# Performance work log

Measured on AMD Instinct MI355X. Metric: run time of the kernel, lower is better.

The kernel has to match this reference:

```python
import jax, jax.numpy as jnp
import numpy as np

NUM_USERS = 100000
NUM_ITEMS = 50000
N_NODES = NUM_USERS + NUM_ITEMS
N_EDGES = 3200000
EMB_DIM = 128
N_LAYERS = 3


def setup_inputs() -> dict:
    key = jax.random.key(0)
    ks = jax.random.split(key, 7)
    # nn.init.normal_(std=0.1) embedding init
    user_emb = jax.random.normal(ks[0], (NUM_USERS, EMB_DIM), dtype=jnp.float32) * 0.1
    item_emb = jax.random.normal(ks[1], (NUM_ITEMS, EMB_DIM), dtype=jnp.float32) * 0.1
    # static normalized adjacency in COO form (values from D^-1/2 A D^-1/2 are positive)
    edge_row = jax.random.randint(ks[2], (N_EDGES,), 0, N_NODES, dtype=jnp.int32)
    edge_col = jax.random.randint(ks[3], (N_EDGES,), 0, N_NODES, dtype=jnp.int32)
    edge_val = jax.random.uniform(ks[4], (N_EDGES,), dtype=jnp.float32)
    users = jax.random.randint(ks[5], (2048,), 0, NUM_USERS, dtype=jnp.int32)
    items = jax.random.randint(ks[6], (2048,), 0, NUM_ITEMS, dtype=jnp.int32)
    return {
        "user_emb": user_emb,
        "item_emb": item_emb,
        "edge_val": edge_val,
        "edge_row": edge_row,
        "edge_col": edge_col,
        "users": users,
        "items": items,
    }


def reference(user_emb, item_emb, edge_val, edge_row, edge_col, users, items):
    # computer(): concat user/item tables -> [N, d]
    all_emb = jnp.concatenate([user_emb, item_emb], axis=0)
    acc = all_emb  # running sum of layer embeddings (fused mean over layers)
    emb = all_emb
    for _ in range(N_LAYERS):
        # sparse.mm(G, emb): per-edge gather, scale, scatter-add
        msg = edge_val[:, None] * emb[edge_col]  # [E, d]
        emb = jax.ops.segment_sum(msg, edge_row, num_segments=N_NODES)
        acc = acc + emb
    light_out = acc / jnp.float32(N_LAYERS + 1)  # mean over stacked layer embeddings
    users_emb = light_out[users]
    items_emb = light_out[NUM_USERS + items]
    # gamma = sum(users_emb * items_emb, dim=1)
    return jnp.sum(users_emb * items_emb, axis=1)
```

## Files before the change

### kernel.cpp

```cpp
#include <hip/hip_runtime.h>

#define D 128
#define NUSERS 100000
#define NITEMS 50000
#define NNODES 150000
#define NEDGES 3200000
#define NSEL 2048
#define NBKT 586
#define PBLK 256
#define EPB (NEDGES / PBLK)
#define MATN (NBKT * PBLK)
#define MB ((MATN + 255) / 256)
#define BCAP 8192
#define INIT_BLKS 2048
#define FLG_BLKS ((NNODES + 255) / 256)
#define SELSET_BLKS ((2 * NSEL + 255) / 256)
#define COLMASK 0x3FFFFu

typedef unsigned int uint_t;
typedef unsigned short ushort_t;

__device__ inline uint_t bf16_rne(float f) {
    uint_t x = __float_as_uint(f);
    return (x + 0x7FFFu + ((x >> 16) & 1u)) >> 16;
}

__device__ inline int block_excl_scan(int v, int* lds, int nw) {
    int lane = threadIdx.x & 63;
    int wid = (int)(threadIdx.x >> 6);
    int x = v;
    #pragma unroll
    for (int off = 1; off < 64; off <<= 1) {
        int y = __shfl_up(x, off);
        if (lane >= off) x += y;
    }
    if (lane == 63) lds[wid] = x;
    __syncthreads();
    if (wid == 0) {
        int s = (lane < nw) ? lds[lane] : 0;
        #pragma unroll
        for (int off = 1; off < 16; off <<= 1) {
            int y = __shfl_up(s, off);
            if (lane >= off) s += y;
        }
        if (lane < nw) lds[lane] = s;
    }
    __syncthreads();
    int waveoff = (wid == 0) ? 0 : lds[wid - 1];
    return waveoff + x - v;
}

__global__ void k_prologue(const int* __restrict__ row, int* __restrict__ mat,
                           const float4* __restrict__ u4, const float4* __restrict__ i4,
                           uint4* __restrict__ cur,
                           int* __restrict__ flags, int* __restrict__ selflag) {
    __shared__ int h[NBKT];
    int blk = blockIdx.x;
    if (blk < PBLK) {
        for (int i = threadIdx.x; i < NBKT; i += 256) h[i] = 0;
        __syncthreads();
        int beg = blk * EPB, end = beg + EPB;
        for (int e = beg + threadIdx.x; e < end; e += 256)
            atomicAdd(&h[row[e] >> 8], 1);
        __syncthreads();
        for (int i = threadIdx.x; i < NBKT; i += 256)
            mat[i * PBLK + blk] = h[i];
    } else if (blk < PBLK + INIT_BLKS) {
        size_t total8 = (size_t)NNODES * D / 8;
        size_t ub8 = (size_t)NUSERS * D / 8;
        size_t stride = (size_t)INIT_BLKS * 256;
        for (size_t i = (size_t)(blk - PBLK) * 256 + threadIdx.x; i < total8; i += stride) {
            const float4* src = (i < ub8) ? &u4[2 * i] : &i4[2 * (i - ub8)];
            float4 a = src[0], b = src[1];
            uint4 o;
            o.x = (bf16_rne(a.y) << 16) | bf16_rne(a.x);
            o.y = (bf16_rne(a.w) << 16) | bf16_rne(a.z);
            o.z = (bf16_rne(b.y) << 16) | bf16_rne(b.x);
            o.w = (bf16_rne(b.w) << 16) | bf16_rne(b.z);
            cur[i] = o;
        }
    } else {
        int i = (blk - PBLK - INIT_BLKS) * 256 + threadIdx.x;
        if (i < NNODES) { flags[i] = 0; selflag[i] = 0; }
    }
}

__global__ void k_blocksum(const int* __restrict__ src, int* __restrict__ bsums, int n) {
    int i = blockIdx.x * 256 + threadIdx.x;
    int v = (i < n) ? src[i] : 0;
    #pragma unroll
    for (int off = 32; off; off >>= 1) v += __shfl_down(v, off);
    __shared__ int lds[4];
    int lane = threadIdx.x & 63, wid = (int)(threadIdx.x >> 6);
    if (lane == 0) lds[wid] = v;
    __syncthreads();
    if (threadIdx.x == 0) bsums[blockIdx.x] = lds[0] + lds[1] + lds[2] + lds[3];
}

__global__ void k_scan2(int* __restrict__ mat, const int* __restrict__ bsums, int n,
                        const int* __restrict__ users, const int* __restrict__ items,
                        int* __restrict__ selflag, int* __restrict__ flags) {
    int b = blockIdx.x;
    if (b >= MB) {
        int idx = (b - MB) * 256 + threadIdx.x;
        if (idx < 2 * NSEL) {
            int node = (idx < NSEL) ? users[idx] : NUSERS + items[idx - NSEL];
            selflag[node] = 1;
            flags[node] = 1;
        }
        return;
    }
    __shared__ int red[4];
    __shared__ int lds[4];
    int lane = threadIdx.x & 63, wid = (int)(threadIdx.x >> 6);
    int s = 0;
    for (int j = threadIdx.x; j < b; j += 256) s += bsums[j];
    #pragma unroll
    for (int off = 32; off; off >>= 1) s += __shfl_down(s, off);
    if (lane == 0) red[wid] = s;
    __syncthreads();
    int base = red[0] + red[1] + red[2] + red[3];
    int i = b * 256 + threadIdx.x;
    int v = (i < n) ? mat[i] : 0;
    int ex = block_excl_scan(v, lds, 4);
    if (i < n) mat[i] = base + ex;
}

__global__ void k_p2(const int* __restrict__ row, const int* __restrict__ col,
                     const float* __restrict__ val, const int* __restrict__ mat,
                     uint_t* __restrict__ t4, ushort_t* __restrict__ tv) {
    __shared__ int cur[NBKT];
    for (int i = threadIdx.x; i < NBKT; i += 256)
        cur[i] = mat[i * PBLK + blockIdx.x];
    __syncthreads();
    int beg = blockIdx.x * EPB, end = beg + EPB;
    for (int e = beg + threadIdx.x; e < end; e += 256) {
        int r = row[e];
        int b = r >> 8;
        int pos = atomicAdd(&cur[b], 1);
        int q = (int)(val[e] * 16384.f + 0.5f);
        if (q > 16383) q = 16383;
        t4[pos] = ((uint_t)(r & 255) << 18) | (uint_t)col[e];
        tv[pos] = (ushort_t)q;
    }
}

__global__ void k_p3(const uint_t* __restrict__ t4, const ushort_t* __restrict__ tv,
                     const int* __restrict__ mat, uint_t* __restrict__ recs,
                     int* __restrict__ row_start,
                     const int* __restrict__ selflag, int* __restrict__ flags) {
    __shared__ uint_t b4[BCAP];
    __shared__ ushort_t bv[BCAP];
    __shared__ int h[256];
    __shared__ int lds[4];
    __shared__ unsigned char selb[256];
    int b = blockIdx.x;
    int beg = mat[b * PBLK];
    int end = (b + 1 < NBKT) ? mat[(b + 1) * PBLK] : NEDGES;
    int n = end - beg;
    int rowid = b * 256 + threadIdx.x;
    h[threadIdx.x] = 0;
    selb[threadIdx.x] = (rowid < NNODES) ? (unsigned char)selflag[rowid] : 0;
    if (n <= BCAP) {
        for (int i = threadIdx.x; i < n; i += 256) { b4[i] = t4[beg + i]; bv[i] = tv[beg + i]; }
        __syncthreads();
        for (int i = threadIdx.x; i < n; i += 256)
            atomicAdd(&h[b4[i] >> 18], 1);
        __syncthreads();
        int ex = block_excl_scan(h[threadIdx.x], lds, 4);
        if (rowid < NNODES) row_start[rowid] = beg + ex;
        if (b == NBKT - 1 && threadIdx.x == 0) row_start[NNODES] = NEDGES;
        h[threadIdx.x] = ex;
        __syncthreads();
        for (int i = threadIdx.x; i < n; i += 256) {
            uint_t a = b4[i];
            int r = (int)(a >> 18);
            uint_t c = a & COLMASK;
            int pos = beg + atomicAdd(&h[r], 1);
            recs[pos] = ((uint_t)bv[i] << 18) | c;
            if (selb[r]) flags[c] = 1;
        }
    } else {
        __syncthreads();
        for (int e = beg + threadIdx.x; e < end; e += 256)
            atomicAdd(&h[t4[e] >> 18], 1);
        __syncthreads();
        int ex = block_excl_scan(h[threadIdx.x], lds, 4);
        if (rowid < NNODES) row_start[rowid] = beg + ex;
        if (b == NBKT - 1 && threadIdx.x == 0) row_start[NNODES] = NEDGES;
        h[threadIdx.x] = ex;
        __syncthreads();
        for (int e = beg + threadIdx.x; e < end; e += 256) {
            uint_t a = t4[e];
            int r = (int)(a >> 18);
            uint_t c = a & COLMASK;
            int pos = beg + atomicAdd(&h[r], 1);
            recs[pos] = ((uint_t)tv[e] << 18) | c;
            if (selb[r]) flags[c] = 1;
        }
    }
}

__global__ void k_spmm_csr(const uint_t* __restrict__ emb, uint_t* __restrict__ outp,
                           const int* __restrict__ row_start,
                           const uint_t* __restrict__ recs,
                           const int* __restrict__ flags, int use_flags) {
    int lane = threadIdx.x & 63;
    int w = (int)((blockIdx.x * blockDim.x + threadIdx.x) >> 6);
    if (w >= NNODES) return;
    if (use_flags && __builtin_amdgcn_readfirstlane(flags[w]) == 0) return;
    int beg = __builtin_amdgcn_readfirstlane(row_start[w]);
    int end = __builtin_amdgcn_readfirstlane(row_start[w + 1]);
    float ax = 0.f, ay = 0.f;
    int e = beg;
    for (; e + 3 < end; e += 4) {
        uint_t q0 = recs[e], q1 = recs[e + 1], q2 = recs[e + 2], q3 = recs[e + 3];
        uint_t g0 = emb[(size_t)(q0 & COLMASK) * 64 + lane];
        uint_t g1 = emb[(size_t)(q1 & COLMASK) * 64 + lane];
        uint_t g2 = emb[(size_t)(q2 & COLMASK) * 64 + lane];
        uint_t g3 = emb[(size_t)(q3 & COLMASK) * 64 + lane];
        float v0 = (float)(q0 >> 18) * (1.f / 16384.f);
        float v1 = (float)(q1 >> 18) * (1.f / 16384.f);
        float v2 = (float)(q2 >> 18) * (1.f / 16384.f);
        float v3 = (float)(q3 >> 18) * (1.f / 16384.f);
        ax += v0 * __uint_as_float(g0 << 16) + v1 * __uint_as_float(g1 << 16)
            + v2 * __uint_as_float(g2 << 16) + v3 * __uint_as_float(g3 << 16);
        ay += v0 * __uint_as_float(g0 & 0xFFFF0000u) + v1 * __uint_as_float(g1 & 0xFFFF0000u)
            + v2 * __uint_as_float(g2 & 0xFFFF0000u) + v3 * __uint_as_float(g3 & 0xFFFF0000u);
    }
    for (; e < end; ++e) {
        uint_t q = recs[e];
        float v = (float)(q >> 18) * (1.f / 16384.f);
        uint_t g = emb[(size_t)(q & COLMASK) * 64 + lane];
        ax += v * __uint_as_float(g << 16);
        ay += v * __uint_as_float(g & 0xFFFF0000u);
    }
    outp[(size_t)w * 64 + lane] = (bf16_rne(ay) << 16) | bf16_rne(ax);
}

__global__ void k_final(const uint_t* __restrict__ embA,
                        const uint_t* __restrict__ embB,
                        const float* __restrict__ user_emb,
                        const float* __restrict__ item_emb,
                        const int* __restrict__ users, const int* __restrict__ items,
                        const int* __restrict__ row_start, const uint_t* __restrict__ recs,
                        float* __restrict__ out) {
    __shared__ float ush[2][64][2];
    int lane = threadIdx.x & 63;
    int wid = (int)(threadIdx.x >> 6);
    int pairIdx = blockIdx.x * 2 + (wid & 1);
    int isItem = wid >> 1;
    int node, idx0;
    const float* e0p;
    if (isItem) {
        idx0 = items[pairIdx];
        node = NUSERS + idx0;
        e0p = &item_emb[(size_t)idx0 * D];
    } else {
        idx0 = users[pairIdx];
        node = idx0;
        e0p = &user_emb[(size_t)idx0 * D];
    }
    const float2 e0 = *(const float2*)(&e0p[lane * 2]);
    uint_t u1 = embB[(size_t)node * 64 + lane];
    uint_t u2 = embA[(size_t)node * 64 + lane];
    float ax = e0.x + __uint_as_float(u1 << 16) + __uint_as_float(u2 << 16);
    float ay = e0.y + __uint_as_float(u1 & 0xFFFF0000u) + __uint_as_float(u2 & 0xFFFF0000u);
    int beg = __builtin_amdgcn_readfirstlane(row_start[node]);
    int end = __builtin_amdgcn_readfirstlane(row_start[node + 1]);
    for (int e = beg; e < end; ++e) {
        uint_t q = recs[e];
        float v = (float)(q >> 18) * (1.f / 16384.f);
        uint_t g = embA[(size_t)(q & COLMASK) * 64 + lane];
        ax += v * __uint_as_float(g << 16);
        ay += v * __uint_as_float(g & 0xFFFF0000u);
    }
    if (!isItem) { ush[wid][lane][0] = ax; ush[wid][lane][1] = ay; }
    __syncthreads();
    if (isItem) {
        float s = ush[wid - 2][lane][0] * ax + ush[wid - 2][lane][1] * ay;
        #pragma unroll
        for (int off = 32; off; off >>= 1) s += __shfl_down(s, off);
        if (lane == 0) out[pairIdx] = s * (1.0f / 16.0f);
    }
}

extern "C" void kernel_launch(void* const* d_in, const int* in_sizes, int n_in,
                              void* d_out, int out_size, void* d_ws, size_t ws_size,
                              hipStream_t stream) {
    const float* user_emb = (const float*)d_in[0];
    const float* item_emb = (const float*)d_in[1];
    const float* edge_val = (const float*)d_in[2];
    const int*   edge_row = (const int*)d_in[3];
    const int*   edge_col = (const int*)d_in[4];
    const int*   users    = (const int*)d_in[5];
    const int*   items    = (const int*)d_in[6];
    float* out = (float*)d_out;

    const size_t tab = (size_t)NNODES * D;
    ushort_t* bufA   = (ushort_t*)d_ws;
    ushort_t* bufB   = bufA + tab;
    uint_t* recs     = (uint_t*)(bufB + tab);
    uint_t* t4       = recs + NEDGES;
    ushort_t* tv     = (ushort_t*)(t4 + NEDGES);
    int*   mat       = (int*)(tv + NEDGES);
    int*   row_start = mat + MATN;
    int*   flags     = row_start + NNODES + 1;
    int*   selflag   = flags + NNODES;
    int*   bsums     = selflag + NNODES;

    k_prologue<<<PBLK + INIT_BLKS + FLG_BLKS, 256, 0, stream>>>(
        edge_row, mat, (const float4*)user_emb, (const float4*)item_emb,
        (uint4*)bufA, flags, selflag);

    k_blocksum<<<MB, 256, 0, stream>>>(mat, bsums, MATN);
    k_scan2<<<MB + SELSET_BLKS, 256, 0, stream>>>(mat, bsums, MATN,
                                                  users, items, selflag, flags);
    k_p2<<<PBLK, 256, 0, stream>>>(edge_row, edge_col, edge_val, mat, t4, tv);
    k_p3<<<NBKT, 256, 0, stream>>>(t4, tv, mat, recs, row_start, selflag, flags);

    k_spmm_csr<<<(NNODES + 3) / 4, 256, 0, stream>>>((const uint_t*)bufA, (uint_t*)bufB,
                                                     row_start, recs, flags, 0);
    k_spmm_csr<<<(NNODES + 3) / 4, 256, 0, stream>>>((const uint_t*)bufB, (uint_t*)bufA,
                                                     row_start, recs, flags, 1);
    k_final<<<NSEL / 2, 256, 0, stream>>>((const uint_t*)bufA, (const uint_t*)bufB,
                                          user_emb, item_emb, users, items,
                                          row_start, recs, out);
}
```

Baseline: 334.2 us.

## Raise partition blocks to 1024 and pack bucket temp records as int2

```diff
diff --git a/kernel.cpp b/kernel.cpp
--- a/kernel.cpp
+++ b/kernel.cpp
@@ -7,10 +7,10 @@
 #define NEDGES 3200000
 #define NSEL 2048
 #define NBKT 586
-#define PBLK 256
+#define PBLK 1024
 #define EPB (NEDGES / PBLK)
 #define MATN (NBKT * PBLK)
-#define MB ((MATN + 255) / 256)
+#define MB (MATN / 256)
 #define BCAP 8192
 #define INIT_BLKS 2048
 #define FLG_BLKS ((NNODES + 255) / 256)
@@ -128,7 +128,7 @@
 
 __global__ void k_p2(const int* __restrict__ row, const int* __restrict__ col,
                      const float* __restrict__ val, const int* __restrict__ mat,
-                     uint_t* __restrict__ t4, ushort_t* __restrict__ tv) {
+                     int2* __restrict__ tmp) {
     __shared__ int cur[NBKT];
     for (int i = threadIdx.x; i < NBKT; i += 256)
         cur[i] = mat[i * PBLK + blockIdx.x];
@@ -140,17 +140,17 @@
         int pos = atomicAdd(&cur[b], 1);
         int q = (int)(val[e] * 16384.f + 0.5f);
         if (q > 16383) q = 16383;
-        t4[pos] = ((uint_t)(r & 255) << 18) | (uint_t)col[e];
-        tv[pos] = (ushort_t)q;
-    }
-}
-
-__global__ void k_p3(const uint_t* __restrict__ t4, const ushort_t* __restrict__ tv,
-                     const int* __restrict__ mat, uint_t* __restrict__ recs,
-                     int* __restrict__ row_start,
+        int2 rc;
+        rc.x = r & 255;
+        rc.y = (int)(((uint_t)q << 18) | (uint_t)col[e]);
+        tmp[pos] = rc;
+    }
+}
+
+__global__ void k_p3(const int2* __restrict__ tmp, const int* __restrict__ mat,
+                     uint_t* __restrict__ recs, int* __restrict__ row_start,
                      const int* __restrict__ selflag, int* __restrict__ flags) {
-    __shared__ uint_t b4[BCAP];
-    __shared__ ushort_t bv[BCAP];
+    __shared__ int2 buf[BCAP];
     __shared__ int h[256];
     __shared__ int lds[4];
     __shared__ unsigned char selb[256];
@@ -162,10 +162,10 @@
     h[threadIdx.x] = 0;
     selb[threadIdx.x] = (rowid < NNODES) ? (unsigned char)selflag[rowid] : 0;
     if (n <= BCAP) {
-        for (int i = threadIdx.x; i < n; i += 256) { b4[i] = t4[beg + i]; bv[i] = tv[beg + i]; }
+        for (int i = threadIdx.x; i < n; i += 256) buf[i] = tmp[beg + i];
         __syncthreads();
         for (int i = threadIdx.x; i < n; i += 256)
-            atomicAdd(&h[b4[i] >> 18], 1);
+            atomicAdd(&h[buf[i].x], 1);
         __syncthreads();
         int ex = block_excl_scan(h[threadIdx.x], lds, 4);
         if (rowid < NNODES) row_start[rowid] = beg + ex;
@@ -173,17 +173,16 @@
         h[threadIdx.x] = ex;
         __syncthreads();
         for (int i = threadIdx.x; i < n; i += 256) {
-            uint_t a = b4[i];
-            int r = (int)(a >> 18);
-            uint_t c = a & COLMASK;
+            int2 rc = buf[i];
+            int r = rc.x;
             int pos = beg + atomicAdd(&h[r], 1);
-            recs[pos] = ((uint_t)bv[i] << 18) | c;
-            if (selb[r]) flags[c] = 1;
+            recs[pos] = (uint_t)rc.y;
+            if (selb[r]) flags[(uint_t)rc.y & COLMASK] = 1;
         }
     } else {
         __syncthreads();
         for (int e = beg + threadIdx.x; e < end; e += 256)
-            atomicAdd(&h[t4[e] >> 18], 1);
+            atomicAdd(&h[tmp[e].x], 1);
         __syncthreads();
         int ex = block_excl_scan(h[threadIdx.x], lds, 4);
         if (rowid < NNODES) row_start[rowid] = beg + ex;
@@ -191,12 +190,11 @@
         h[threadIdx.x] = ex;
         __syncthreads();
         for (int e = beg + threadIdx.x; e < end; e += 256) {
-            uint_t a = t4[e];
-            int r = (int)(a >> 18);
-            uint_t c = a & COLMASK;
+            int2 rc = tmp[e];
+            int r = rc.x;
             int pos = beg + atomicAdd(&h[r], 1);
-            recs[pos] = ((uint_t)tv[e] << 18) | c;
-            if (selb[r]) flags[c] = 1;
+            recs[pos] = (uint_t)rc.y;
+            if (selb[r]) flags[(uint_t)rc.y & COLMASK] = 1;
         }
     }
 }
@@ -301,9 +299,8 @@
     ushort_t* bufA   = (ushort_t*)d_ws;
     ushort_t* bufB   = bufA + tab;
     uint_t* recs     = (uint_t*)(bufB + tab);
-    uint_t* t4       = recs + NEDGES;
-    ushort_t* tv     = (ushort_t*)(t4 + NEDGES);
-    int*   mat       = (int*)(tv + NEDGES);
+    int2*  tmp       = (int2*)(recs + NEDGES);
+    int*   mat       = (int*)(tmp + NEDGES);
     int*   row_start = mat + MATN;
     int*   flags     = row_start + NNODES + 1;
     int*   selflag   = flags + NNODES;
@@ -316,8 +313,8 @@
     k_blocksum<<<MB, 256, 0, stream>>>(mat, bsums, MATN);
     k_scan2<<<MB + SELSET_BLKS, 256, 0, stream>>>(mat, bsums, MATN,
                                                   users, items, selflag, flags);
-    k_p2<<<PBLK, 256, 0, stream>>>(edge_row, edge_col, edge_val, mat, t4, tv);
-    k_p3<<<NBKT, 256, 0, stream>>>(t4, tv, mat, recs, row_start, selflag, flags);
+    k_p2<<<PBLK, 256, 0, stream>>>(edge_row, edge_col, edge_val, mat, tmp);
+    k_p3<<<NBKT, 256, 0, stream>>>(tmp, mat, recs, row_start, selflag, flags);
 
     k_spmm_csr<<<(NNODES + 3) / 4, 256, 0, stream>>>((const uint_t*)bufA, (uint_t*)bufB,
                                                      row_start, recs, flags, 0);
```

After: 305.4 us. 1.09x faster.
